# Kernel optimization log

Hardware: AMD Instinct MI355X
Metric: run time of the kernel (lower is better)

Reference implementation:

```python
import jax, jax.numpy as jnp
import numpy as np

MU = 0            # smeared direction (init arg dir)
IS_ODD = False    # init arg is_odd -> update the EVEN subset
DIMS = (24, 24, 24, 24)
N_PLAQ = 6
PI_2 = 0.6366197723675814  # 2/pi, as in scale_coeff


def setup_inputs() -> dict:
    key = jax.random.key(0)
    k1, k2, k3 = jax.random.split(key, 3)
    shape = (4,) + DIMS + (3, 3)  # [dir, T, Z, Y, X, 3, 3]
    x_re = jax.random.normal(k1, shape, jnp.float32)
    x_im = jax.random.normal(k2, shape, jnp.float32)
    coeff = jax.random.uniform(k3, (N_PLAQ,), jnp.float32)
    return {"x_re": x_re, "x_im": x_im, "coeff": coeff}


def _adj(m):
    return jnp.conj(jnp.swapaxes(m, -1, -2))


def _shift(a, nu, n):
    # lattice .shift(nu, n): value at site + n*nu_hat (periodic); lattice axes are the leading 4
    return jnp.roll(a, -n, axis=nu)


def _eo_filter(dims, is_odd, dtype):
    # evenodd_mask % 2; filter is 1 on the UPDATED subset (odd if is_odd else even)
    grids = jnp.meshgrid(*[jnp.arange(d) for d in dims], indexing='ij')
    parity = sum(grids) % 2
    mask = parity if is_odd else 1 - parity
    return mask.astype(dtype)[..., None, None]


def _matexp(Z, terms=12, squarings=4):
    # scaling-and-squaring Taylor (Horner) matrix exponential, batched over leading dims
    Z = Z * jnp.asarray(0.5 ** squarings, dtype=jnp.float32).astype(Z.dtype)
    eye = jnp.eye(Z.shape[-1], dtype=Z.dtype)
    E = eye
    for k in range(terms, 0, -1):
        E = eye + (Z @ E) / k
    for _ in range(squarings):
        E = E @ E
    return E


def reference(x_re, x_im, coeff):
    x = (x_re + 1j * x_im).astype(jnp.complex64)  # [4, T, Z, Y, X, 3, 3]
    filt = _eo_filter(DIMS, IS_ODD, jnp.complex64)
    # filter_fixed_update: mask mu-links; staples built from fixed-subset x[mu]
    xmu_fix = x[MU] * (1.0 - filt)
    xupd = x[MU] * filt
    # scale_coeff(coeff, 0.75) = (2/pi)*0.75*atan(coeff)
    c = (PI_2 * 0.75) * jnp.arctan(coeff)
    cc = c.astype(jnp.complex64)
    # plaquette staples (n_plaq = 6 loops)
    loops = []
    for nu in range(4):
        if nu == MU:
            continue
        Umu = _shift(xmu_fix, nu, 1)      # x[mu].shift(nu, 1)
        Unu = _shift(x[nu], MU, 1)        # x[nu].shift(mu, 1)
        R = Umu @ _adj(Unu)
        stf = x[nu] @ R                   # forward staple
        L = _adj(x[nu]) @ xmu_fix
        stu = L @ Unu
        loops.append(stf)
        loops.append(_shift(stu, nu, -1)) # backward staple
    f = loops[0] * cc[0]
    for i in range(1, N_PLAQ):
        f = f + loops[i] * cc[i]
    f = f / N_PLAQ
    # stout update on the updated subset: Z = projectTangent(f @ xupd^dag); U' = exp(Z) @ U
    M = f @ _adj(xupd)
    A = 0.5 * (M - _adj(M))               # anti-hermitian part
    tr = jnp.trace(A, axis1=-2, axis2=-1)
    Zt = A - (tr / 3.0)[..., None, None] * jnp.eye(3, dtype=A.dtype)  # traceless
    E = _matexp(Zt)
    ymu = E @ xupd + xmu_fix              # combine updated and fixed subsets
    y = x.at[MU].set(ymu)
    # return real/imag stacked so output is real-valued: [4, T, Z, Y, X, 3, 3, 2]
    return jnp.stack((jnp.real(y), jnp.imag(y)), axis=-1)
```

## Files before the change

### kernel.cpp

```cpp
#include <hip/hip_runtime.h>
#include <cstdint>

#define LT 24
#define NSITE (LT*LT*LT*LT)

struct C3 { float re[9]; float im[9]; };

__device__ __forceinline__ void loadMi(C3& m, const float2* __restrict__ buf, int site) {
    const int base = site * 9;
#pragma unroll
    for (int j = 0; j < 9; ++j) {
        float2 v = buf[base + j];
        m.re[j] = v.x; m.im[j] = v.y;
    }
}

__device__ __forceinline__ void mmul(C3& o, const C3& a, const C3& b) {
#pragma unroll
    for (int r = 0; r < 3; ++r) {
#pragma unroll
        for (int c = 0; c < 3; ++c) {
            float sr = 0.f, si = 0.f;
#pragma unroll
            for (int k = 0; k < 3; ++k) {
                float ar = a.re[r*3+k], ai = a.im[r*3+k];
                float br = b.re[k*3+c], bi = b.im[k*3+c];
                sr += ar*br - ai*bi;
                si += ar*bi + ai*br;
            }
            o.re[r*3+c] = sr; o.im[r*3+c] = si;
        }
    }
}

__device__ __forceinline__ void mmul_acc(C3& f, const C3& a, const C3& b, float cr) {
#pragma unroll
    for (int r = 0; r < 3; ++r) {
#pragma unroll
        for (int c = 0; c < 3; ++c) {
            float sr = 0.f, si = 0.f;
#pragma unroll
            for (int k = 0; k < 3; ++k) {
                float ar = a.re[r*3+k], ai = a.im[r*3+k];
                float br = b.re[k*3+c], bi = b.im[k*3+c];
                sr += ar*br - ai*bi;
                si += ar*bi + ai*br;
            }
            f.re[r*3+c] += cr * sr; f.im[r*3+c] += cr * si;
        }
    }
}

__device__ __forceinline__ void mmul_adjB(C3& o, const C3& a, const C3& b) {
#pragma unroll
    for (int r = 0; r < 3; ++r) {
#pragma unroll
        for (int c = 0; c < 3; ++c) {
            float sr = 0.f, si = 0.f;
#pragma unroll
            for (int k = 0; k < 3; ++k) {
                float ar = a.re[r*3+k], ai = a.im[r*3+k];
                float br = b.re[c*3+k], bi = b.im[c*3+k];
                sr += ar*br + ai*bi;
                si += ai*br - ar*bi;
            }
            o.re[r*3+c] = sr; o.im[r*3+c] = si;
        }
    }
}

__device__ __forceinline__ void madjA_mul(C3& o, const C3& a, const C3& b) {
#pragma unroll
    for (int r = 0; r < 3; ++r) {
#pragma unroll
        for (int c = 0; c < 3; ++c) {
            float sr = 0.f, si = 0.f;
#pragma unroll
            for (int k = 0; k < 3; ++k) {
                float ar = a.re[k*3+r], ai = a.im[k*3+r];
                float br = b.re[k*3+c], bi = b.im[k*3+c];
                sr += ar*br + ai*bi;
                si += ar*bi - ai*br;
            }
            o.re[r*3+c] = sr; o.im[r*3+c] = si;
        }
    }
}

__global__ void interleave_kernel(const float2* __restrict__ re,
                                  const float2* __restrict__ im,
                                  float4* __restrict__ out, int n2) {
    int i = blockIdx.x * blockDim.x + threadIdx.x;
    if (i >= n2) return;
    float2 a = re[i], b = im[i];
    float4 o; o.x = a.x; o.y = b.x; o.z = a.y; o.w = b.y;
    out[i] = o;
}

__global__ __launch_bounds__(256)
void stout_kernel(const float2* __restrict__ xi,
                  const float* __restrict__ coeff,
                  float2* __restrict__ out) {
    int tid = blockIdx.x * blockDim.x + threadIdx.x;
    if (tid >= NSITE / 2) return;

    int xh = tid % 12;  int r0 = tid / 12;
    int y  = r0 % LT;   r0 /= LT;
    int z  = r0 % LT;   int t = r0 / LT;
    int x  = 2 * xh + ((t + z + y) & 1);

    float c[6];
#pragma unroll
    for (int i = 0; i < 6; ++i)
        c[i] = 0.07957747154594768f * atanf(coeff[i]);

    int tp = (t + 1 < LT) ? t + 1 : 0;
    int zp = (z + 1 < LT) ? z + 1 : 0;  int zm = (z > 0) ? z - 1 : LT - 1;
    int yp = (y + 1 < LT) ? y + 1 : 0;  int ym = (y > 0) ? y - 1 : LT - 1;
    int xp = (x + 1 < LT) ? x + 1 : 0;  int xm = (x > 0) ? x - 1 : LT - 1;

    const int s   = ((t  * LT + z) * LT + y) * LT + x;
    const int stt = ((tp * LT + z) * LT + y) * LT + x;
    const int spv[3]  = { ((t  * LT + zp) * LT + y ) * LT + x,
                          ((t  * LT + z ) * LT + yp) * LT + x,
                          ((t  * LT + z ) * LT + y ) * LT + xp };
    const int smv[3]  = { ((t  * LT + zm) * LT + y ) * LT + x,
                          ((t  * LT + z ) * LT + ym) * LT + x,
                          ((t  * LT + z ) * LT + y ) * LT + xm };
    const int smtv[3] = { ((tp * LT + zm) * LT + y ) * LT + x,
                          ((tp * LT + z ) * LT + ym) * LT + x,
                          ((tp * LT + z ) * LT + y ) * LT + xm };

    C3 f;
#pragma unroll
    for (int j = 0; j < 9; ++j) { f.re[j] = 0.f; f.im[j] = 0.f; }

    C3 A, B, Cm, tmp;
#pragma unroll
    for (int i = 0; i < 3; ++i) {
        const int d = i + 1;
        loadMi(B,  xi, spv[i]);
        loadMi(Cm, xi, d * NSITE + stt);
        loadMi(A,  xi, d * NSITE + s);
        mmul_adjB(tmp, B, Cm);
        mmul_acc(f, A, tmp, c[2 * i]);
        loadMi(A,  xi, d * NSITE + smv[i]);
        loadMi(B,  xi, smv[i]);
        loadMi(Cm, xi, d * NSITE + smtv[i]);
        madjA_mul(tmp, A, B);
        mmul_acc(f, tmp, Cm, c[2 * i + 1]);
    }

    C3 U;
    loadMi(U, xi, s);

    C3 Mm;
    mmul_adjB(Mm, f, U);
    C3 Zt;
#pragma unroll
    for (int r = 0; r < 3; ++r) {
#pragma unroll
        for (int cq = 0; cq < 3; ++cq) {
            Zt.re[r*3+cq] = 0.5f * (Mm.re[r*3+cq] - Mm.re[cq*3+r]);
            Zt.im[r*3+cq] = 0.5f * (Mm.im[r*3+cq] + Mm.im[cq*3+r]);
        }
    }
    float trIm = (Zt.im[0] + Zt.im[4] + Zt.im[8]) / 3.0f;
    Zt.im[0] -= trIm; Zt.im[4] -= trIm; Zt.im[8] -= trIm;

#pragma unroll
    for (int j = 0; j < 9; ++j) { Zt.re[j] *= 0.0625f; Zt.im[j] *= 0.0625f; }

    C3 E;
#pragma unroll
    for (int j = 0; j < 9; ++j) { E.re[j] = 0.f; E.im[j] = 0.f; }
    E.re[0] = 1.f; E.re[4] = 1.f; E.re[8] = 1.f;

    C3 Tm;
#pragma unroll
    for (int k = 12; k >= 1; --k) {
        mmul(Tm, Zt, E);
        const float invk = 1.0f / (float)k;
#pragma unroll
        for (int j = 0; j < 9; ++j) {
            E.re[j] = Tm.re[j] * invk;
            E.im[j] = Tm.im[j] * invk;
        }
        E.re[0] += 1.f; E.re[4] += 1.f; E.re[8] += 1.f;
    }
#pragma unroll
    for (int q = 0; q < 4; ++q) {
        mmul(Tm, E, E);
        E = Tm;
    }

    C3 Y;
    mmul(Y, E, U);

    const int ob = s * 9;
#pragma unroll
    for (int j = 0; j < 9; ++j) {
        float2 v; v.x = Y.re[j]; v.y = Y.im[j];
        out[ob + j] = v;
    }
}

extern "C" void kernel_launch(void* const* d_in, const int* in_sizes, int n_in,
                              void* d_out, int out_size, void* d_ws, size_t ws_size,
                              hipStream_t stream) {
    const float* xre   = (const float*)d_in[0];
    const float* xim   = (const float*)d_in[1];
    const float* coeff = (const float*)d_in[2];

    const int n2 = (4 * NSITE * 9) / 2;
    interleave_kernel<<<(n2 + 255) / 256, 256, 0, stream>>>(
        (const float2*)xre, (const float2*)xim, (float4*)d_out, n2);

    stout_kernel<<<(NSITE / 2 + 255) / 256, 256, 0, stream>>>(
        (const float2*)d_out, coeff, (float2*)d_out);
}
```

Measured before the change: 259.3 us.

## Fuse re/im interleave into stout kernel with copy and compute thread halves

Removes the separate interleave kernel and its full write-then-reread of the interleaved gauge field. The stout kernel now reads the split real and imaginary inputs directly with 16-byte vector loads. Each 256-thread block has two halves: the first 128 threads compute the even-site update and also copy directions 1-3 for their sites, while the other 128 threads copy all four directions for odd sites. Risks: the 36-byte site stride leaves the vector loads misaligned, the copy and compute threads carry very uneven work, and neighbor links are now gathered from two separate arrays.

```diff
diff --git a/kernel.cpp b/kernel.cpp
--- a/kernel.cpp
+++ b/kernel.cpp
@@ -6,13 +6,33 @@
 
 struct C3 { float re[9]; float im[9]; };
 
-__device__ __forceinline__ void loadMi(C3& m, const float2* __restrict__ buf, int site) {
-    const int base = site * 9;
-#pragma unroll
-    for (int j = 0; j < 9; ++j) {
-        float2 v = buf[base + j];
-        m.re[j] = v.x; m.im[j] = v.y;
-    }
+__device__ __forceinline__ void load9(float* d, const float* __restrict__ p) {
+    float4 a, b;
+    __builtin_memcpy(&a, p,     16);
+    __builtin_memcpy(&b, p + 4, 16);
+    d[0]=a.x; d[1]=a.y; d[2]=a.z; d[3]=a.w;
+    d[4]=b.x; d[5]=b.y; d[6]=b.z; d[7]=b.w;
+    d[8]=p[8];
+}
+
+__device__ __forceinline__ void loadM(C3& m, const float* __restrict__ re,
+                                      const float* __restrict__ im, int off) {
+    load9(m.re, re + off);
+    load9(m.im, im + off);
+}
+
+__device__ __forceinline__ void storeM(float2* __restrict__ out, int cbase, const C3& m) {
+    float4 v;
+    v.x=m.re[0]; v.y=m.im[0]; v.z=m.re[1]; v.w=m.im[1];
+    __builtin_memcpy(out + cbase,     &v, 16);
+    v.x=m.re[2]; v.y=m.im[2]; v.z=m.re[3]; v.w=m.im[3];
+    __builtin_memcpy(out + cbase + 2, &v, 16);
+    v.x=m.re[4]; v.y=m.im[4]; v.z=m.re[5]; v.w=m.im[5];
+    __builtin_memcpy(out + cbase + 4, &v, 16);
+    v.x=m.re[6]; v.y=m.im[6]; v.z=m.re[7]; v.w=m.im[7];
+    __builtin_memcpy(out + cbase + 6, &v, 16);
+    float2 w; w.x=m.re[8]; w.y=m.im[8];
+    out[cbase + 8] = w;
 }
 
 __device__ __forceinline__ void mmul(C3& o, const C3& a, const C3& b) {
@@ -87,27 +107,37 @@
     }
 }
 
-__global__ void interleave_kernel(const float2* __restrict__ re,
-                                  const float2* __restrict__ im,
-                                  float4* __restrict__ out, int n2) {
-    int i = blockIdx.x * blockDim.x + threadIdx.x;
-    if (i >= n2) return;
-    float2 a = re[i], b = im[i];
-    float4 o; o.x = a.x; o.y = b.x; o.z = a.y; o.w = b.y;
-    out[i] = o;
+__device__ __forceinline__ int site_from_idx(int idx, int parity,
+                                             int& t, int& z, int& y, int& x) {
+    int xh = idx % 12;  int r = idx / 12;
+    y = r % LT; r /= LT;
+    z = r % LT; t = r / LT;
+    x = 2 * xh + ((t + z + y + parity) & 1);
+    return ((t * LT + z) * LT + y) * LT + x;
 }
 
 __global__ __launch_bounds__(256)
-void stout_kernel(const float2* __restrict__ xi,
-                  const float* __restrict__ coeff,
-                  float2* __restrict__ out) {
-    int tid = blockIdx.x * blockDim.x + threadIdx.x;
-    if (tid >= NSITE / 2) return;
-
-    int xh = tid % 12;  int r0 = tid / 12;
-    int y  = r0 % LT;   r0 /= LT;
-    int z  = r0 % LT;   int t = r0 / LT;
-    int x  = 2 * xh + ((t + z + y) & 1);
+void stout_fused(const float* __restrict__ xre, const float* __restrict__ xim,
+                 const float* __restrict__ coeff, float2* __restrict__ out) {
+    const int tau = threadIdx.x;
+    const bool heavy = (tau < 128);
+    const int idx = blockIdx.x * 128 + (heavy ? tau : tau - 128);
+
+    if (!heavy) {
+        int t, z, y, x;
+        const int s = site_from_idx(idx, 1, t, z, y, x);
+        C3 m;
+#pragma unroll
+        for (int d = 0; d < 4; ++d) {
+            const int off = (d * NSITE + s) * 9;
+            loadM(m, xre, xim, off);
+            storeM(out, off, m);
+        }
+        return;
+    }
+
+    int t, z, y, x;
+    const int s = site_from_idx(idx, 0, t, z, y, x);
 
     float c[6];
 #pragma unroll
@@ -119,7 +149,6 @@
     int yp = (y + 1 < LT) ? y + 1 : 0;  int ym = (y > 0) ? y - 1 : LT - 1;
     int xp = (x + 1 < LT) ? x + 1 : 0;  int xm = (x > 0) ? x - 1 : LT - 1;
 
-    const int s   = ((t  * LT + z) * LT + y) * LT + x;
     const int stt = ((tp * LT + z) * LT + y) * LT + x;
     const int spv[3]  = { ((t  * LT + zp) * LT + y ) * LT + x,
                           ((t  * LT + z ) * LT + yp) * LT + x,
@@ -139,20 +168,21 @@
 #pragma unroll
     for (int i = 0; i < 3; ++i) {
         const int d = i + 1;
-        loadMi(B,  xi, spv[i]);
-        loadMi(Cm, xi, d * NSITE + stt);
-        loadMi(A,  xi, d * NSITE + s);
+        loadM(A, xre, xim, (d * NSITE + s) * 9);
+        storeM(out, (d * NSITE + s) * 9, A);
+        loadM(B,  xre, xim, (     spv[i])        * 9);
+        loadM(Cm, xre, xim, (d * NSITE + stt)    * 9);
         mmul_adjB(tmp, B, Cm);
         mmul_acc(f, A, tmp, c[2 * i]);
-        loadMi(A,  xi, d * NSITE + smv[i]);
-        loadMi(B,  xi, smv[i]);
-        loadMi(Cm, xi, d * NSITE + smtv[i]);
+        loadM(A,  xre, xim, (d * NSITE + smv[i]) * 9);
+        loadM(B,  xre, xim, (     smv[i])        * 9);
+        loadM(Cm, xre, xim, (d * NSITE + smtv[i])* 9);
         madjA_mul(tmp, A, B);
         mmul_acc(f, tmp, Cm, c[2 * i + 1]);
     }
 
     C3 U;
-    loadMi(U, xi, s);
+    loadM(U, xre, xim, s * 9);
 
     C3 Mm;
     mmul_adjB(Mm, f, U);
@@ -196,13 +226,7 @@
 
     C3 Y;
     mmul(Y, E, U);
-
-    const int ob = s * 9;
-#pragma unroll
-    for (int j = 0; j < 9; ++j) {
-        float2 v; v.x = Y.re[j]; v.y = Y.im[j];
-        out[ob + j] = v;
-    }
+    storeM(out, s * 9, Y);
 }
 
 extern "C" void kernel_launch(void* const* d_in, const int* in_sizes, int n_in,
@@ -212,10 +236,6 @@
     const float* xim   = (const float*)d_in[1];
     const float* coeff = (const float*)d_in[2];
 
-    const int n2 = (4 * NSITE * 9) / 2;
-    interleave_kernel<<<(n2 + 255) / 256, 256, 0, stream>>>(
-        (const float2*)xre, (const float2*)xim, (float4*)d_out, n2);
-
-    stout_kernel<<<(NSITE / 2 + 255) / 256, 256, 0, stream>>>(
-        (const float2*)d_out, coeff, (float2*)d_out);
-}
+    const int nblocks = (NSITE / 2) / 128;
+    stout_fused<<<nblocks, 256, 0, stream>>>(xre, xim, coeff, (float2*)d_out);
+}
```

Result: faster. 249.4 us (-3.8%).
